# Kernel tuning notes

Measured on AMD Instinct MI355X. Metric: run time of the kernel, lower is better.

The kernel has to match this reference:

```python
import jax, jax.numpy as jnp
import numpy as np

N_NODES = 20000
N_EDGES = 640000
FEAT = 128


def setup_inputs() -> dict:
    key = jax.random.key(0)
    k1, k2, k3, k4 = jax.random.split(key, 4)
    x = jax.random.normal(k1, (1, N_NODES, FEAT, 4), dtype=jnp.float32)
    edge_index = jax.random.randint(k2, (2, N_EDGES), 0, N_NODES, dtype=jnp.int64)
    # Linear(in_channels=128, out_channels=128): W [out, in], b [out]
    W = jax.random.normal(k3, (FEAT, FEAT), dtype=jnp.float32) * 0.05
    b = jax.random.normal(k4, (FEAT,), dtype=jnp.float32) * 0.05
    return {"x": x, "edge_index": edge_index, "W": W, "b": b}


def reference(x, edge_index, W, b):
    # x: [B, N, F, T]
    B, N, F, T = x.shape
    # permute -> [B, T, N, F]; Linear over feature dim (out == in == F)
    h = jnp.einsum('bnft,of->btno', x, W) + b          # [B, T, N, F]
    h = h.reshape(B * T, N, F)                          # flatten batch*time
    src = edge_index[0]  # message source (x_j)
    dst = edge_index[1]  # scatter target
    msgs = h[:, src, :]                                 # [B*T, E, F] gather
    # scatter-max per target node (PyG aggr='max'); vmap over batch*time
    agg = jax.vmap(lambda m: jax.ops.segment_max(m, dst, num_segments=N))(msgs)
    # nodes with no incoming edges: segment_max yields -inf -> 0 (PyG fill)
    agg = jnp.where(jnp.isneginf(agg), jnp.zeros_like(agg), agg)
    out = agg.reshape(B, T, N, F).transpose(0, 2, 3, 1)  # [B, N, F, T]
    return out
```

## Files before the change

### kernel.cpp

```cpp
#include <hip/hip_runtime.h>
#include <hip/hip_bf16.h>
#include <stdint.h>

#define N_NODES 20000
#define N_EDGES 640000
#define FEAT 128
#define CAPD 128
#define NPHASE 8

typedef __attribute__((ext_vector_type(8))) short bf16x8;
typedef __attribute__((ext_vector_type(4))) float f32x4;

__device__ __forceinline__ unsigned pkbf16(float lo, float hi) {
  __hip_bfloat162 p = __float22bfloat162_rn(make_float2(lo, hi));
  return *reinterpret_cast<unsigned*>(&p);
}

__device__ __forceinline__ unsigned short enc16(float f) {
  unsigned a = __float_as_uint(f);
  unsigned b = (a + 0x7FFFu + ((a >> 16) & 1u)) >> 16;
  unsigned s = (unsigned)((int)a >> 31);
  return (unsigned short)((b ^ 0x8000u) ^ (s & 0x7FFFu));
}

__device__ __forceinline__ float dec16(unsigned e) {
  unsigned b = (e & 0x8000u) ? (e ^ 0x8000u) : (e ^ 0xFFFFu);
  return __uint_as_float(b << 16);
}

__device__ __forceinline__ void pmax(unsigned& a, unsigned v) {
  asm("v_pk_max_u16 %0, %0, %1" : "+v"(a) : "v"(v));
}

#define PMX4(v)                                              \
  do {                                                       \
    pmax(a0, (v).x); pmax(a1, (v).y);                        \
    pmax(a2, (v).z); pmax(a3, (v).w);                        \
  } while (0)

__global__ void init_kernel(const float* __restrict__ W,
                            unsigned short* __restrict__ Wbf,
                            int* __restrict__ cnt) {
  int i = blockIdx.x * 256 + threadIdx.x;
  if (i < N_NODES) cnt[i] = 0;
  if (i < FEAT * FEAT / 2) {
    float2 w = ((const float2*)W)[i];
    ((unsigned*)Wbf)[i] = pkbf16(w.x, w.y);
  }
}

__global__ __launch_bounds__(256) void scatter_kernel(const int* __restrict__ ei,
                                                      int* __restrict__ cnt,
                                                      unsigned short* __restrict__ csr) {
  int e = blockIdx.x * 256 + threadIdx.x;
  int src = ei[e];
  int dst = ei[N_EDGES + e];
  int pos = atomicAdd(&cnt[dst], 1);
  if (pos < CAPD) csr[(size_t)dst * CAPD + pos] = (unsigned short)src;
}

__global__ __launch_bounds__(256) void gemm_kernel(
    const float4* __restrict__ x, const unsigned short* __restrict__ Wbf,
    const float* __restrict__ b, uint4* __restrict__ h) {
  __shared__ __align__(16) unsigned short sm[17408 / 2];
  const int tid = threadIdx.x;
  const int n0 = blockIdx.x * 16;

#pragma unroll
  for (int it = 0; it < 4; ++it) {
    int e = tid + it * 256;
    int n = e >> 6, fp = e & 63;
    float4 a = x[(size_t)(n0 + n) * 128 + 2 * fp];
    float4 c = x[(size_t)(n0 + n) * 128 + 2 * fp + 1];
    ((unsigned*)sm)[(0 * 16 + n) * 68 + fp] = pkbf16(a.x, c.x);
    ((unsigned*)sm)[(1 * 16 + n) * 68 + fp] = pkbf16(a.y, c.y);
    ((unsigned*)sm)[(2 * 16 + n) * 68 + fp] = pkbf16(a.z, c.z);
    ((unsigned*)sm)[(3 * 16 + n) * 68 + fp] = pkbf16(a.w, c.w);
  }

  __syncthreads();

  const int wv = tid >> 6;
  const int l = tid & 63;
  const int col = l & 15;
  const int quad = l >> 4;

  f32x4 acc[8];
#pragma unroll
  for (int os = 0; os < 8; ++os) {
    float bv = b[os * 16 + col];
    acc[os] = (f32x4){bv, bv, bv, bv};
  }

#pragma unroll
  for (int k = 0; k < 4; ++k) {
    bf16x8 af = *(const bf16x8*)&sm[(wv * 16 + col) * 136 + k * 32 + quad * 8];
#pragma unroll
    for (int os = 0; os < 8; ++os) {
      bf16x8 bfv = *(const bf16x8*)&Wbf[(os * 16 + col) * 128 + k * 32 + quad * 8];
      acc[os] = __builtin_amdgcn_mfma_f32_16x16x32_bf16(af, bfv, acc[os], 0, 0, 0);
    }
  }

  __syncthreads();

#pragma unroll
  for (int os = 0; os < 8; ++os) {
#pragma unroll
    for (int r = 0; r < 4; ++r) {
      sm[(quad * 4 + r) * 520 + (os * 16 + col) * 4 + wv] = enc16(acc[os][r]);
    }
  }
  __syncthreads();

#pragma unroll
  for (int it = 0; it < 4; ++it) {
    int e = tid + it * 256;
    int n = e >> 6, q = e & 63;
    uint4 v = *(const uint4*)&sm[n * 520 + q * 8];
    h[(size_t)(n0 + n) * 64 + q] = v;
  }
}

__global__ __launch_bounds__(256) void agg_kernel(
    const uint4* __restrict__ h, const int* __restrict__ cnt,
    const unsigned short* __restrict__ csr, float4* __restrict__ out) {
  const int bid = blockIdx.x;
  const int p = bid & 7;
  const int grp = bid >> 3;
  const int w = threadIdx.x >> 6;
  const int lane = threadIdx.x & 63;
  const int n = grp * 4 + w;
  const int sub = lane >> 3;
  const int oq = lane & 7;

  int e1 = (int)csr[(size_t)n * CAPD + lane];
  int e2 = (int)csr[(size_t)n * CAPD + 64 + lane];
  int deg = cnt[n];
  deg = deg > CAPD ? CAPD : deg;
  int idx0 = __shfl(e1, 0);

  unsigned a0 = 0x007F007Fu, a1 = a0, a2 = a0, a3 = a0;

  const size_t pbase = (size_t)p * 8 + oq;
  int ngrp = (deg + 7) >> 3;
  int g = 0;
  for (; g + 2 <= ngrp; g += 2) {
    int s0 = g * 8 + sub;
    int s1 = s0 + 8;
    int srcA = __shfl((g < 8) ? e1 : e2, s0 & 63);
    int srcB = __shfl((g + 1 < 8) ? e1 : e2, s1 & 63);
    srcA = (s0 < deg) ? srcA : idx0;
    srcB = (s1 < deg) ? srcB : idx0;
    uint4 vA = h[(size_t)srcA * 64 + pbase];
    uint4 vB = h[(size_t)srcB * 64 + pbase];
    PMX4(vA);
    PMX4(vB);
  }
  if (g < ngrp) {
    int s0 = g * 8 + sub;
    int src = __shfl((g < 8) ? e1 : e2, s0 & 63);
    src = (s0 < deg) ? src : idx0;
    uint4 v = h[(size_t)src * 64 + pbase];
    PMX4(v);
  }

#pragma unroll
  for (int d = 8; d <= 32; d <<= 1) {
    pmax(a0, (unsigned)__shfl_xor((int)a0, d));
    pmax(a1, (unsigned)__shfl_xor((int)a1, d));
    pmax(a2, (unsigned)__shfl_xor((int)a2, d));
    pmax(a3, (unsigned)__shfl_xor((int)a3, d));
  }

  if (lane < 8) {
    float4 o0, o1;
    if (deg == 0) {
      o0 = make_float4(0.f, 0.f, 0.f, 0.f);
      o1 = o0;
    } else {
      o0 = make_float4(dec16(a0 & 0xFFFFu), dec16(a0 >> 16),
                       dec16(a1 & 0xFFFFu), dec16(a1 >> 16));
      o1 = make_float4(dec16(a2 & 0xFFFFu), dec16(a2 >> 16),
                       dec16(a3 & 0xFFFFu), dec16(a3 >> 16));
    }
    out[(size_t)n * 128 + p * 16 + lane * 2] = o0;
    out[(size_t)n * 128 + p * 16 + lane * 2 + 1] = o1;
  }
}

extern "C" void kernel_launch(void* const* d_in, const int* in_sizes, int n_in,
                              void* d_out, int out_size, void* d_ws, size_t ws_size,
                              hipStream_t stream) {
  const float* x = (const float*)d_in[0];
  const int* ei = (const int*)d_in[1];
  const float* W = (const float*)d_in[2];
  const float* b = (const float*)d_in[3];
  float* out = (float*)d_out;

  char* ws = (char*)d_ws;
  uint4* h = (uint4*)ws;
  int* cnt = (int*)(ws + 20480000);
  unsigned short* csr = (unsigned short*)(ws + 20560000);
  unsigned short* Wbf = (unsigned short*)(ws + 25680000);

  init_kernel<<<(N_NODES + 255) / 256, 256, 0, stream>>>(W, Wbf, cnt);
  scatter_kernel<<<N_EDGES / 256, 256, 0, stream>>>(ei, cnt, csr);
  gemm_kernel<<<N_NODES / 16, 256, 0, stream>>>((const float4*)x, Wbf, b, h);
  agg_kernel<<<(N_NODES / 4) * NPHASE, 256, 0, stream>>>(h, cnt, csr, (float4*)out);
}
```

Baseline: 203.9 us.

## Permute CSR slot layout so each lane loads its neighbor indices as one vector

The scatter kernel now writes neighbor indices into a permuted slot order, so each 8-lane subgroup's indices sit contiguously. The aggregation kernel then fetches them with one 16-byte load per lane instead of two 2-byte loads followed by a shuffle for every neighbor group. The gather loop is fully unrolled, with degree thresholds at 32/48/64/96, and each gather uses 32-bit offset arithmetic. This removes per-iteration shuffles and loop overhead. In exchange, lanes may issue loads for inactive slots, which are redirected to the first neighbor, and code size grows.

```diff
diff --git a/kernel.cpp b/kernel.cpp
--- a/kernel.cpp
+++ b/kernel.cpp
@@ -51,12 +51,15 @@
 
 __global__ __launch_bounds__(256) void scatter_kernel(const int* __restrict__ ei,
                                                       int* __restrict__ cnt,
-                                                      unsigned short* __restrict__ csr) {
+                                                      unsigned short* __restrict__ csrT) {
   int e = blockIdx.x * 256 + threadIdx.x;
   int src = ei[e];
   int dst = ei[N_EDGES + e];
   int pos = atomicAdd(&cnt[dst], 1);
-  if (pos < CAPD) csr[(size_t)dst * CAPD + pos] = (unsigned short)src;
+  if (pos < CAPD) {
+    int tp = (pos & 64) | ((pos & 7) << 3) | ((pos >> 3) & 7);
+    csrT[(size_t)dst * CAPD + tp] = (unsigned short)src;
+  }
 }
 
 __global__ __launch_bounds__(256) void gemm_kernel(
@@ -124,7 +127,7 @@
 
 __global__ __launch_bounds__(256) void agg_kernel(
     const uint4* __restrict__ h, const int* __restrict__ cnt,
-    const unsigned short* __restrict__ csr, float4* __restrict__ out) {
+    const unsigned short* __restrict__ csrT, float4* __restrict__ out) {
   const int bid = blockIdx.x;
   const int p = bid & 7;
   const int grp = bid >> 3;
@@ -134,35 +137,58 @@
   const int sub = lane >> 3;
   const int oq = lane & 7;
 
-  int e1 = (int)csr[(size_t)n * CAPD + lane];
-  int e2 = (int)csr[(size_t)n * CAPD + 64 + lane];
   int deg = cnt[n];
   deg = deg > CAPD ? CAPD : deg;
-  int idx0 = __shfl(e1, 0);
+
+  const char* cb = (const char*)csrT + (size_t)n * 256 + sub * 16;
+  uint4 ia = *(const uint4*)cb;
 
   unsigned a0 = 0x007F007Fu, a1 = a0, a2 = a0, a3 = a0;
 
-  const size_t pbase = (size_t)p * 8 + oq;
-  int ngrp = (deg + 7) >> 3;
-  int g = 0;
-  for (; g + 2 <= ngrp; g += 2) {
-    int s0 = g * 8 + sub;
-    int s1 = s0 + 8;
-    int srcA = __shfl((g < 8) ? e1 : e2, s0 & 63);
-    int srcB = __shfl((g + 1 < 8) ? e1 : e2, s1 & 63);
-    srcA = (s0 < deg) ? srcA : idx0;
-    srcB = (s1 < deg) ? srcB : idx0;
-    uint4 vA = h[(size_t)srcA * 64 + pbase];
-    uint4 vB = h[(size_t)srcB * 64 + pbase];
-    PMX4(vA);
-    PMX4(vB);
-  }
-  if (g < ngrp) {
-    int s0 = g * 8 + sub;
-    int src = __shfl((g < 8) ? e1 : e2, s0 & 63);
-    src = (s0 < deg) ? src : idx0;
-    uint4 v = h[(size_t)src * 64 + pbase];
-    PMX4(v);
+  const char* hb = (const char*)h;
+  const unsigned pb = (((unsigned)p * 8 + oq) << 4);
+
+#define GETLO(wrd) ((int)((wrd) & 0xFFFFu))
+#define GETHI(wrd) ((int)((wrd) >> 16))
+#define LDS4(iv, idv, I)                                          \
+  {                                                               \
+    int id_ = ((I)*8 + sub < deg) ? (idv) : idx0;                 \
+    iv = *(const uint4*)(hb + (((unsigned)id_ << 10) + pb));      \
+  }
+
+  if (deg > 0) {
+    int idx0 = __shfl(GETLO(ia.x), 0);
+    uint4 v0, v1, v2, v3;
+    LDS4(v0, GETLO(ia.x), 0);
+    LDS4(v1, GETHI(ia.x), 1);
+    LDS4(v2, GETLO(ia.y), 2);
+    LDS4(v3, GETHI(ia.y), 3);
+    PMX4(v0); PMX4(v1); PMX4(v2); PMX4(v3);
+    if (deg > 32) {
+      LDS4(v0, GETLO(ia.z), 4);
+      LDS4(v1, GETHI(ia.z), 5);
+      PMX4(v0); PMX4(v1);
+      if (deg > 48) {
+        LDS4(v2, GETLO(ia.w), 6);
+        LDS4(v3, GETHI(ia.w), 7);
+        PMX4(v2); PMX4(v3);
+      }
+    }
+    if (deg > 64) {
+      uint4 ib = *(const uint4*)(cb + 128);
+      LDS4(v0, GETLO(ib.x), 8);
+      LDS4(v1, GETHI(ib.x), 9);
+      LDS4(v2, GETLO(ib.y), 10);
+      LDS4(v3, GETHI(ib.y), 11);
+      PMX4(v0); PMX4(v1); PMX4(v2); PMX4(v3);
+      if (deg > 96) {
+        LDS4(v0, GETLO(ib.z), 12);
+        LDS4(v1, GETHI(ib.z), 13);
+        LDS4(v2, GETLO(ib.w), 14);
+        LDS4(v3, GETHI(ib.w), 15);
+        PMX4(v0); PMX4(v1); PMX4(v2); PMX4(v3);
+      }
+    }
   }
 
 #pragma unroll
@@ -201,11 +227,11 @@
   char* ws = (char*)d_ws;
   uint4* h = (uint4*)ws;
   int* cnt = (int*)(ws + 20480000);
-  unsigned short* csr = (unsigned short*)(ws + 20560000);
+  unsigned short* csrT = (unsigned short*)(ws + 20560000);
   unsigned short* Wbf = (unsigned short*)(ws + 25680000);
 
   init_kernel<<<(N_NODES + 255) / 256, 256, 0, stream>>>(W, Wbf, cnt);
-  scatter_kernel<<<N_EDGES / 256, 256, 0, stream>>>(ei, cnt, csr);
+  scatter_kernel<<<N_EDGES / 256, 256, 0, stream>>>(ei, cnt, csrT);
   gemm_kernel<<<N_NODES / 16, 256, 0, stream>>>((const float4*)x, Wbf, b, h);
-  agg_kernel<<<(N_NODES / 4) * NPHASE, 256, 0, stream>>>(h, cnt, csr, (float4*)out);
-}
+  agg_kernel<<<(N_NODES / 4) * NPHASE, 256, 0, stream>>>(h, cnt, csrT, (float4*)out);
+}
```

New measurement: 201.1 us. About the same (-1.4%).

## Map eight nodes per wave in aggregation and fold W conversion into scatter

Applied to the files above, without the earlier changes.

The aggregation kernel now gives each 8-lane group its own destination node, so a wave handles 8 nodes instead of one. Each lane walks its node's neighbor list serially, which removes the cross-lane shuffles and the final reduction. The loop runs to the wave's maximum degree, so lanes with smaller degree reload a duplicate neighbor. The init kernel is replaced by a memset, and the W-to-bf16 conversion is folded into the scatter kernel, which saves one launch.

```diff
diff --git a/kernel.cpp b/kernel.cpp
--- a/kernel.cpp
+++ b/kernel.cpp
@@ -38,23 +38,18 @@
     pmax(a2, (v).z); pmax(a3, (v).w);                        \
   } while (0)
 
-__global__ void init_kernel(const float* __restrict__ W,
-                            unsigned short* __restrict__ Wbf,
-                            int* __restrict__ cnt) {
-  int i = blockIdx.x * 256 + threadIdx.x;
-  if (i < N_NODES) cnt[i] = 0;
-  if (i < FEAT * FEAT / 2) {
-    float2 w = ((const float2*)W)[i];
-    ((unsigned*)Wbf)[i] = pkbf16(w.x, w.y);
-  }
-}
-
 __global__ __launch_bounds__(256) void scatter_kernel(const int* __restrict__ ei,
                                                       int* __restrict__ cnt,
-                                                      unsigned short* __restrict__ csr) {
-  int e = blockIdx.x * 256 + threadIdx.x;
-  int src = ei[e];
-  int dst = ei[N_EDGES + e];
+                                                      unsigned short* __restrict__ csr,
+                                                      const float* __restrict__ W,
+                                                      unsigned short* __restrict__ Wbf) {
+  int t = blockIdx.x * 256 + threadIdx.x;
+  if (t < FEAT * FEAT / 2) {
+    float2 w = ((const float2*)W)[t];
+    ((unsigned*)Wbf)[t] = pkbf16(w.x, w.y);
+  }
+  int src = ei[t];
+  int dst = ei[N_EDGES + t];
   int pos = atomicAdd(&cnt[dst], 1);
   if (pos < CAPD) csr[(size_t)dst * CAPD + pos] = (unsigned short)src;
 }
@@ -130,63 +125,47 @@
   const int grp = bid >> 3;
   const int w = threadIdx.x >> 6;
   const int lane = threadIdx.x & 63;
-  const int n = grp * 4 + w;
-  const int sub = lane >> 3;
+  const int g = lane >> 3;
   const int oq = lane & 7;
+  const int n = grp * 32 + w * 8 + g;
 
-  int e1 = (int)csr[(size_t)n * CAPD + lane];
-  int e2 = (int)csr[(size_t)n * CAPD + 64 + lane];
   int deg = cnt[n];
   deg = deg > CAPD ? CAPD : deg;
-  int idx0 = __shfl(e1, 0);
+
+  const unsigned short* cs = csr + (size_t)n * CAPD;
+  int idx0 = (deg > 0) ? (int)cs[0] : 0;
+
+  int dmax = deg;
+#pragma unroll
+  for (int d = 8; d <= 32; d <<= 1) {
+    int o = __shfl_xor(dmax, d);
+    dmax = o > dmax ? o : dmax;
+  }
+  dmax = __builtin_amdgcn_readfirstlane(dmax);
 
   unsigned a0 = 0x007F007Fu, a1 = a0, a2 = a0, a3 = a0;
+  const char* hb = (const char*)h;
+  const unsigned pb = (((unsigned)p * 8 + oq) << 4);
 
-  const size_t pbase = (size_t)p * 8 + oq;
-  int ngrp = (deg + 7) >> 3;
-  int g = 0;
-  for (; g + 2 <= ngrp; g += 2) {
-    int s0 = g * 8 + sub;
-    int s1 = s0 + 8;
-    int srcA = __shfl((g < 8) ? e1 : e2, s0 & 63);
-    int srcB = __shfl((g + 1 < 8) ? e1 : e2, s1 & 63);
-    srcA = (s0 < deg) ? srcA : idx0;
-    srcB = (s1 < deg) ? srcB : idx0;
-    uint4 vA = h[(size_t)srcA * 64 + pbase];
-    uint4 vB = h[(size_t)srcB * 64 + pbase];
-    PMX4(vA);
-    PMX4(vB);
-  }
-  if (g < ngrp) {
-    int s0 = g * 8 + sub;
-    int src = __shfl((g < 8) ? e1 : e2, s0 & 63);
-    src = (s0 < deg) ? src : idx0;
-    uint4 v = h[(size_t)src * 64 + pbase];
+#pragma unroll 2
+  for (int j = 0; j < dmax; ++j) {
+    int id = (j < deg) ? (int)cs[j] : idx0;
+    uint4 v = *(const uint4*)(hb + (((unsigned)id << 10) + pb));
     PMX4(v);
   }
 
-#pragma unroll
-  for (int d = 8; d <= 32; d <<= 1) {
-    pmax(a0, (unsigned)__shfl_xor((int)a0, d));
-    pmax(a1, (unsigned)__shfl_xor((int)a1, d));
-    pmax(a2, (unsigned)__shfl_xor((int)a2, d));
-    pmax(a3, (unsigned)__shfl_xor((int)a3, d));
+  float4 o0, o1;
+  if (deg == 0) {
+    o0 = make_float4(0.f, 0.f, 0.f, 0.f);
+    o1 = o0;
+  } else {
+    o0 = make_float4(dec16(a0 & 0xFFFFu), dec16(a0 >> 16),
+                     dec16(a1 & 0xFFFFu), dec16(a1 >> 16));
+    o1 = make_float4(dec16(a2 & 0xFFFFu), dec16(a2 >> 16),
+                     dec16(a3 & 0xFFFFu), dec16(a3 >> 16));
   }
-
-  if (lane < 8) {
-    float4 o0, o1;
-    if (deg == 0) {
-      o0 = make_float4(0.f, 0.f, 0.f, 0.f);
-      o1 = o0;
-    } else {
-      o0 = make_float4(dec16(a0 & 0xFFFFu), dec16(a0 >> 16),
-                       dec16(a1 & 0xFFFFu), dec16(a1 >> 16));
-      o1 = make_float4(dec16(a2 & 0xFFFFu), dec16(a2 >> 16),
-                       dec16(a3 & 0xFFFFu), dec16(a3 >> 16));
-    }
-    out[(size_t)n * 128 + p * 16 + lane * 2] = o0;
-    out[(size_t)n * 128 + p * 16 + lane * 2 + 1] = o1;
-  }
+  out[(size_t)n * 128 + p * 16 + oq * 2] = o0;
+  out[(size_t)n * 128 + p * 16 + oq * 2 + 1] = o1;
 }
 
 extern "C" void kernel_launch(void* const* d_in, const int* in_sizes, int n_in,
@@ -204,8 +183,8 @@
   unsigned short* csr = (unsigned short*)(ws + 20560000);
   unsigned short* Wbf = (unsigned short*)(ws + 25680000);
 
-  init_kernel<<<(N_NODES + 255) / 256, 256, 0, stream>>>(W, Wbf, cnt);
-  scatter_kernel<<<N_EDGES / 256, 256, 0, stream>>>(ei, cnt, csr);
+  hipMemsetAsync(cnt, 0, N_NODES * sizeof(int), stream);
+  scatter_kernel<<<N_EDGES / 256, 256, 0, stream>>>(ei, cnt, csr, W, Wbf);
   gemm_kernel<<<N_NODES / 16, 256, 0, stream>>>((const float4*)x, Wbf, b, h);
-  agg_kernel<<<(N_NODES / 4) * NPHASE, 256, 0, stream>>>(h, cnt, csr, (float4*)out);
+  agg_kernel<<<(N_NODES / 32) * NPHASE, 256, 0, stream>>>(h, cnt, csr, (float4*)out);
 }
```

Measured after the change: 215.2 us. 1.06x slower.
